# Kernel tuning notes

Hardware: AMD Instinct MI355X
Metric: run time of the kernel (lower is better)

Reference implementation:

```python
import jax, jax.numpy as jnp
import numpy as np

T, A, B, N = 16, 64, 64, 12
BATCH, ZS, ENC, DEC = 4096, 100, 400, 400


def setup_inputs() -> dict:
    key = jax.random.key(0)
    ks = jax.random.split(key, 20)
    s = 0.05  # small init so exp(log_sigma)/exp(log_delta) stay well-behaved
    rn = lambda k, shp: s * jax.random.normal(k, shp, dtype=jnp.float32)
    return {
        "x": jax.random.uniform(ks[0], (BATCH, A * B), dtype=jnp.float32),
        "eps": jax.random.normal(ks[1], (T, BATCH, ZS), dtype=jnp.float32),
        # encoder LSTMCell: input = read(2*N*N) concat h_dec(DEC)
        "w_enc_ih": rn(ks[2], (4 * ENC, 2 * N * N + DEC)),
        "w_enc_hh": rn(ks[3], (4 * ENC, ENC)),
        "b_enc_ih": jnp.zeros((4 * ENC,), jnp.float32),
        "b_enc_hh": jnp.zeros((4 * ENC,), jnp.float32),
        # decoder LSTMCell: input = z(ZS)
        "w_dec_ih": rn(ks[4], (4 * DEC, ZS)),
        "w_dec_hh": rn(ks[5], (4 * DEC, DEC)),
        "b_dec_ih": jnp.zeros((4 * DEC,), jnp.float32),
        "b_dec_hh": jnp.zeros((4 * DEC,), jnp.float32),
        "w_mu": rn(ks[6], (ZS, ENC)),
        "b_mu": jnp.zeros((ZS,), jnp.float32),
        "w_sig": rn(ks[7], (ZS, ENC)),
        "b_sig": jnp.zeros((ZS,), jnp.float32),
        "w_attn": rn(ks[8], (5, DEC)),
        "b_attn": jnp.zeros((5,), jnp.float32),
        "w_write": rn(ks[9], (N * N, DEC)),
        "b_write": jnp.zeros((N * N,), jnp.float32),
    }


def _lstm(inp, h, c, wi, wh, bi, bh):
    # PyTorch LSTMCell gate order: i, f, g, o
    g = inp @ wi.T + bi + h @ wh.T + bh
    i, f, gg, o = jnp.split(g, 4, axis=-1)
    c2 = jax.nn.sigmoid(f) * c + jax.nn.sigmoid(i) * jnp.tanh(gg)
    h2 = jax.nn.sigmoid(o) * jnp.tanh(c2)
    return h2, c2


def reference(x, eps, w_enc_ih, w_enc_hh, b_enc_ih, b_enc_hh,
              w_dec_ih, w_dec_hh, b_dec_ih, b_dec_hh,
              w_mu, b_mu, w_sig, b_sig, w_attn, b_attn, w_write, b_write):
    batch = x.shape[0]
    rng = jnp.arange(N, dtype=x.dtype)        # (N,)
    grid_a = jnp.arange(A, dtype=x.dtype)     # (A,)
    grid_b = jnp.arange(B, dtype=x.dtype)     # (B,)
    half = N / 2 + 0.5

    def attn(h_dec):
        p = h_dec @ w_attn.T + b_attn                       # (b,5)
        gx_, gy_, ls2, ld, lg = [p[:, i:i + 1] for i in range(5)]
        gx = (A + 1) / 2 * (gx_ + 1)
        gy = (B + 1) / 2 * (gy_ + 1)
        delta = (max(A, B) - 1) / (N - 1) * jnp.exp(ld)     # (b,1)
        sigma2 = jnp.exp(ls2)[:, :, None]                   # (b,1,1)
        gamma = jnp.exp(lg)                                  # (b,1)
        mu_x = (rng[None, :] - half) * delta + gx            # (b,N)
        mu_y = (rng[None, :] - half) * delta + gy

        def fb(grid, mu):
            t = (grid[None, None, :] - mu[:, :, None]) / (2 * sigma2)
            F = jnp.exp(-t * t)                              # (b,N,len)
            return F / (F.sum(2, keepdims=True) + 1e-9)
        return fb(grid_a, mu_x), fb(grid_b, mu_y), gamma

    def step(carry, eps_t):
        c, h_enc, s_enc, h_dec, s_dec = carry
        x_hat = x - jax.nn.sigmoid(c)
        Fx, Fy, gamma = attn(h_dec)

        def glimpse(img):  # Fy @ img @ Fx^T, scaled by gamma
            g = jnp.einsum('bnB,bBA,bmA->bnm', Fy, img.reshape(-1, B, A), Fx)
            return g.reshape(-1, N * N) * gamma

        r = jnp.concatenate([glimpse(x), glimpse(x_hat)], axis=1)  # (b,2*N*N)
        h_enc, s_enc = _lstm(jnp.concatenate([r, h_dec], axis=1),
                             h_enc, s_enc, w_enc_ih, w_enc_hh, b_enc_ih, b_enc_hh)
        mu = h_enc @ w_mu.T + b_mu
        logsig = h_enc @ w_sig.T + b_sig
        z = mu + jnp.exp(logsig) * eps_t
        h_dec, s_dec = _lstm(z, h_dec, s_dec, w_dec_ih, w_dec_hh, b_dec_ih, b_dec_hh)
        Fx2, Fy2, gamma2 = attn(h_dec)
        w = (h_dec @ w_write.T + b_write).reshape(-1, N, N)
        wr = jnp.einsum('bnB,bnm,bmA->bBA', Fy2, w, Fx2).reshape(-1, A * B) / gamma2
        return (c + wr, h_enc, s_enc, h_dec, s_dec), None

    zf = lambda d: jnp.zeros((batch, d), x.dtype)
    init = (jnp.zeros_like(x), zf(ENC), zf(ENC), zf(DEC), zf(DEC))
    (c, _, _, _, _), _ = jax.lax.scan(step, init, eps)
    return c  # final canvas logits, shape (batch, A*B)
```

## Files before the change

### kernel.cpp

```cpp
#include <hip/hip_runtime.h>
#include <cstdint>
#include <cstddef>

#define T_STEPS 16
#define AA 64
#define BBX 64
#define NF 12
#define BATCH 4096
#define ZS 100
#define ENC 400
#define DEC 400
#define IMG (AA*BBX)
#define RDIM (2*NF*NF)
#define GDIM (4*ENC)

#define KENC 1088
#define KDEC 544
#define KSML 416
#define NBIG 1664
#define NSML 256

typedef __attribute__((ext_vector_type(8))) short bfrag;
typedef __attribute__((ext_vector_type(4))) float f32x4;

__device__ __forceinline__ float sigmoidf_(float v) { return 1.f / (1.f + expf(-v)); }

__device__ __forceinline__ float bf2f(unsigned short u) {
    uint32_t x = ((uint32_t)u) << 16;
    return __builtin_bit_cast(float, x);
}

__device__ __forceinline__ void split2(float f, unsigned short& h, unsigned short& l) {
    uint32_t u = __builtin_bit_cast(uint32_t, f);
    uint32_t hb = (u + 0x7FFFu + ((u >> 16) & 1u)) >> 16;
    float hf = __builtin_bit_cast(float, hb << 16);
    float r = f - hf;
    uint32_t v = __builtin_bit_cast(uint32_t, r);
    uint32_t lb = (v + 0x7FFFu + ((v >> 16) & 1u)) >> 16;
    h = (unsigned short)hb;
    l = (unsigned short)lb;
}

__device__ __forceinline__ void bar_lds() {
    asm volatile("s_waitcnt lgkmcnt(0)" ::: "memory");
    __builtin_amdgcn_s_barrier();
    __builtin_amdgcn_sched_barrier(0);
}

__global__ __launch_bounds__(256, 2) void k_gemm2(
    const unsigned short* __restrict__ Ah, const unsigned short* __restrict__ Al,
    int lda, int a_off,
    const unsigned short* __restrict__ Bh, const unsigned short* __restrict__ Bl,
    int Kpad,
    const float* __restrict__ b1, const float* __restrict__ b2,
    float* __restrict__ C, int NN)
{
    __shared__ unsigned short lA[2][8 * 512];
    __shared__ unsigned short lB[2][8 * 512];

    const int tid = threadIdx.x;
    const int lane = tid & 63;
    const int wave = tid >> 6;
    const int wr = wave >> 1;
    const int wc = wave & 1;
    const int m0 = blockIdx.y * 128;
    const int n0 = blockIdx.x * 128;
    const int rlow = lane & 15;
    const int kg8 = (lane >> 4) * 8;

    const size_t aBase = (size_t)(m0 + rlow) * lda + a_off + kg8;
    const size_t bBase = (size_t)(n0 + rlow) * Kpad + kg8;
    const unsigned short* gsrc;
    unsigned short* ldst;
    size_t stride16;
    if (wave == 0)      { gsrc = Ah + aBase; ldst = &lA[0][0]; stride16 = (size_t)lda * 16; }
    else if (wave == 1) { gsrc = Al + aBase; ldst = &lA[1][0]; stride16 = (size_t)lda * 16; }
    else if (wave == 2) { gsrc = Bh + bBase; ldst = &lB[0][0]; stride16 = (size_t)Kpad * 16; }
    else                { gsrc = Bl + bBase; ldst = &lB[1][0]; stride16 = (size_t)Kpad * 16; }

    f32x4 acc[4][4];
#pragma unroll
    for (int mf = 0; mf < 4; ++mf)
#pragma unroll
        for (int nf = 0; nf < 4; ++nf) acc[mf][nf] = (f32x4){0.f, 0.f, 0.f, 0.f};

    for (int k0 = 0; k0 < Kpad; k0 += 32) {
#pragma unroll
        for (int sub = 0; sub < 8; ++sub) {
            __builtin_amdgcn_global_load_lds(
                (const __attribute__((address_space(1))) void*)(gsrc + (size_t)sub * stride16 + k0),
                (__attribute__((address_space(3))) void*)(ldst + sub * 512), 16, 0, 0);
        }
        __syncthreads();

        bfrag bhf[4], blf[4];
#pragma unroll
        for (int nf = 0; nf < 4; ++nf) {
            bhf[nf] = *(const bfrag*)&lB[0][(wc * 4 + nf) * 512 + lane * 8];
            blf[nf] = *(const bfrag*)&lB[1][(wc * 4 + nf) * 512 + lane * 8];
        }
#pragma unroll
        for (int mf = 0; mf < 4; ++mf) {
            const bfrag ah = *(const bfrag*)&lA[0][(wr * 4 + mf) * 512 + lane * 8];
            const bfrag al = *(const bfrag*)&lA[1][(wr * 4 + mf) * 512 + lane * 8];
#pragma unroll
            for (int nf = 0; nf < 4; ++nf) {
                acc[mf][nf] = __builtin_amdgcn_mfma_f32_16x16x32_bf16(ah, bhf[nf], acc[mf][nf], 0, 0, 0);
                acc[mf][nf] = __builtin_amdgcn_mfma_f32_16x16x32_bf16(ah, blf[nf], acc[mf][nf], 0, 0, 0);
                acc[mf][nf] = __builtin_amdgcn_mfma_f32_16x16x32_bf16(al, bhf[nf], acc[mf][nf], 0, 0, 0);
            }
        }
        __syncthreads();
    }

    const int col = lane & 15;
    const int rowq = (lane >> 4) * 4;
#pragma unroll
    for (int nf = 0; nf < 4; ++nf) {
        const int n = n0 + wc * 64 + nf * 16 + col;
        if (n < NN) {
            float bb = b1[n];
            if (b2) bb += b2[n];
#pragma unroll
            for (int mf = 0; mf < 4; ++mf) {
                const int mbase = m0 + wr * 64 + mf * 16 + rowq;
#pragma unroll
                for (int j = 0; j < 4; ++j)
                    C[(size_t)(mbase + j) * NN + n] = acc[mf][nf][j] + bb;
            }
        }
    }
}

__global__ __launch_bounds__(256) void k_fillw(
    const float* __restrict__ src, int rows, int cols,
    unsigned short* __restrict__ dh, unsigned short* __restrict__ dl,
    int ld, int col0, int row0)
{
    const int i = blockIdx.x * 256 + threadIdx.x;
    if (i >= rows * cols) return;
    const int r = i / cols, c = i - r * cols;
    unsigned short h, l;
    split2(src[i], h, l);
    dh[(size_t)(row0 + r) * ld + col0 + c] = h;
    dl[(size_t)(row0 + r) * ld + col0 + c] = l;
}

__device__ __forceinline__ void attn_compute(
    const float* __restrict__ hd,
    const float* __restrict__ w_attn, const float* __restrict__ b_attn,
    float* __restrict__ p,
    float (* __restrict__ Fx)[68], float (* __restrict__ Fy)[68],
    float* __restrict__ rowinv)
{
    const int t = threadIdx.x;
    const int lane = t & 63, wave = t >> 6;
    for (int o = wave; o < 5; o += 4) {
        float s = 0.f;
        for (int k = lane; k < DEC; k += 64) s += hd[k] * w_attn[o * DEC + k];
#pragma unroll
        for (int off = 32; off; off >>= 1) s += __shfl_down(s, off);
        if (lane == 0) p[o] = s + b_attn[o];
    }
    __syncthreads();
    const float gx = 32.5f * (p[0] + 1.f);
    const float gy = 32.5f * (p[1] + 1.f);
    const float sigma2 = expf(p[2]);
    const float delta = (63.f / 11.f) * expf(p[3]);
    const float inv2s = 1.f / (2.f * sigma2);
    for (int e = t; e < NF * 64; e += 256) {
        const int n = e >> 6, a = e & 63;
        const float mu_x = ((float)n - 6.5f) * delta + gx;
        const float mu_y = ((float)n - 6.5f) * delta + gy;
        const float tx = ((float)a - mu_x) * inv2s;
        const float ty = ((float)a - mu_y) * inv2s;
        Fx[n][a] = expf(-tx * tx);
        Fy[n][a] = expf(-ty * ty);
    }
    __syncthreads();
    for (int rix = wave; rix < 24; rix += 4) {
        const float* row = (rix < 12) ? &Fx[rix][0] : &Fy[rix - 12][0];
        float s = row[lane];
#pragma unroll
        for (int off = 32; off; off >>= 1) s += __shfl_down(s, off);
        if (lane == 0) rowinv[rix] = 1.f / (s + 1e-9f);
    }
    __syncthreads();
    for (int e = t; e < NF * 64; e += 256) {
        const int n = e >> 6, a = e & 63;
        Fx[n][a] *= rowinv[n];
        Fy[n][a] *= rowinv[12 + n];
    }
}

__global__ __launch_bounds__(256) void k_glimpse(
    const float* __restrict__ x, const float* __restrict__ c,
    unsigned short* __restrict__ eAh, unsigned short* __restrict__ eAl,
    const float* __restrict__ w_attn, const float* __restrict__ b_attn)
{
    __shared__ __align__(16) float hd[DEC];
    __shared__ __align__(16) float p[8];
    __shared__ __align__(16) float Fx[NF][68], Fy[NF][68];
    __shared__ __align__(16) float rowinv[24];
    __shared__ __align__(16) float img[IMG], imgh[IMG];
    __shared__ __align__(16) float tmp1[NF][68], tmp2[NF][68];
    const int item = blockIdx.x;
    const int t = threadIdx.x;
    const size_t arow = (size_t)item * KENC;

    for (int i = t; i < DEC; i += 256)
        hd[i] = bf2f(eAh[arow + 288 + i]) + bf2f(eAl[arow + 288 + i]);
    __syncthreads();
    attn_compute(hd, w_attn, b_attn, p, Fx, Fy, rowinv);

    for (int i = t; i < IMG; i += 256) {
        const float xv = x[(size_t)item * IMG + i];
        const float cv = c[(size_t)item * IMG + i];
        img[i] = xv;
        imgh[i] = xv - sigmoidf_(cv);
    }
    __syncthreads();
    const float gamma = expf(p[4]);

    if (t < 192) {
        const int n = t >> 4, a0 = (t & 15) * 4;
        float s10 = 0, s11 = 0, s12 = 0, s13 = 0;
        float s20 = 0, s21 = 0, s22 = 0, s23 = 0;
        for (int Bi = 0; Bi < 64; ++Bi) {
            const float fy = Fy[n][Bi];
            const float4 v1 = *(const float4*)&img[Bi * 64 + a0];
            const float4 v2 = *(const float4*)&imgh[Bi * 64 + a0];
            s10 += fy * v1.x; s11 += fy * v1.y; s12 += fy * v1.z; s13 += fy * v1.w;
            s20 += fy * v2.x; s21 += fy * v2.y; s22 += fy * v2.z; s23 += fy * v2.w;
        }
        *(float4*)&tmp1[n][a0] = make_float4(s10, s11, s12, s13);
        *(float4*)&tmp2[n][a0] = make_float4(s20, s21, s22, s23);
    }
    __syncthreads();

    for (int e = t; e < 2 * NF * NF; e += 256) {
        const int which = e / 144;
        const int idx = e - which * 144;
        const int n = idx / 12, m = idx - (idx / 12) * 12;
        const float (*tp)[68] = which ? tmp2 : tmp1;
        const float4* tv = (const float4*)&tp[n][0];
        const float4* fv = (const float4*)&Fx[m][0];
        float s = 0.f;
#pragma unroll
        for (int a4 = 0; a4 < 16; ++a4) {
            const float4 tvv = tv[a4], fvv = fv[a4];
            s += tvv.x * fvv.x + tvv.y * fvv.y + tvv.z * fvv.z + tvv.w * fvv.w;
        }
        unsigned short vh, vl;
        split2(s * gamma, vh, vl);
        eAh[arow + e] = vh;
        eAl[arow + e] = vl;
    }
}

__global__ __launch_bounds__(256) void k_wrgl(
    const float* __restrict__ x, float* __restrict__ c,
    unsigned short* __restrict__ eAh, unsigned short* __restrict__ eAl,
    const float* __restrict__ w_attn, const float* __restrict__ b_attn,
    const float* __restrict__ wvec)
{
    __shared__ __align__(16) float xx[64][64];
    __shared__ __align__(16) float gg[64][64];
    __shared__ __align__(16) float Fyf[16][68];
    __shared__ __align__(16) float Fx[NF][68];
    __shared__ __align__(16) float tmp[2][NF][68];
    __shared__ __align__(16) float u[64][13];
    __shared__ __align__(16) float hd[DEC];
    __shared__ __align__(16) float p[8];
    __shared__ __align__(16) float rowinv[24];
    __shared__ __align__(16) float wsv[NF * NF];
    const int item = blockIdx.x;
    const int t = threadIdx.x;
    const int lane = t & 63, wave = t >> 6;
    const size_t arow = (size_t)item * KENC;

    float4 cv4[4];
#pragma unroll
    for (int j = 0; j < 4; ++j)
        cv4[j] = *(const float4*)&c[(size_t)item * IMG + j * 1024 + t * 4];
    {
        const float* xsrc = x + (size_t)item * IMG + wave * 1024 + lane * 4;
        float* xdst = &xx[0][0] + wave * 1024;
#pragma unroll
        for (int j = 0; j < 4; ++j)
            __builtin_amdgcn_global_load_lds(
                (const __attribute__((address_space(1))) void*)(xsrc + j * 256),
                (__attribute__((address_space(3))) void*)(xdst + j * 256), 16, 0, 0);
    }
    {
        float hdv0 = bf2f(eAh[arow + 288 + t]) + bf2f(eAl[arow + 288 + t]);
        hd[t] = hdv0;
        if (t + 256 < DEC)
            hd[t + 256] = bf2f(eAh[arow + 288 + t + 256]) + bf2f(eAl[arow + 288 + t + 256]);
        if (t < NF * NF) wsv[t] = wvec[(size_t)item * (NF * NF) + t];
    }
    bar_lds();

    for (int o = wave; o < 5; o += 4) {
        float s = 0.f;
        for (int k = lane; k < DEC; k += 64) s += hd[k] * w_attn[o * DEC + k];
#pragma unroll
        for (int off = 32; off; off >>= 1) s += __shfl_down(s, off);
        if (lane == 0) p[o] = s + b_attn[o];
    }
    bar_lds();
    {
        const float gx = 32.5f * (p[0] + 1.f);
        const float gy = 32.5f * (p[1] + 1.f);
        const float sigma2 = expf(p[2]);
        const float delta = (63.f / 11.f) * expf(p[3]);
        const float inv2s = 1.f / (2.f * sigma2);
        for (int e = t; e < NF * 64; e += 256) {
            const int n = e >> 6, a = e & 63;
            const float mu_x = ((float)n - 6.5f) * delta + gx;
            const float mu_y = ((float)n - 6.5f) * delta + gy;
            const float tx = ((float)a - mu_x) * inv2s;
            const float ty = ((float)a - mu_y) * inv2s;
            Fx[n][a] = expf(-tx * tx);
            Fyf[n][a] = expf(-ty * ty);
        }
        for (int e = t; e < 4 * 68; e += 256)
            Fyf[12 + e / 68][e - (e / 68) * 68] = 0.f;
    }
    bar_lds();
    for (int rix = wave; rix < 24; rix += 4) {
        const float* row = (rix < 12) ? &Fx[rix][0] : &Fyf[rix - 12][0];
        float s = row[lane];
#pragma unroll
        for (int off = 32; off; off >>= 1) s += __shfl_down(s, off);
        if (lane == 0) rowinv[rix] = 1.f / (s + 1e-9f);
    }
    bar_lds();
    for (int e = t; e < NF * 64; e += 256) {
        const int n = e >> 6, a = e & 63;
        Fx[n][a] *= rowinv[n];
        Fyf[n][a] *= rowinv[12 + n];
    }
    bar_lds();
    const float gamma = expf(p[4]);
    const float ginv = 1.f / gamma;
    for (int e = t; e < 64 * NF; e += 256) {
        const int Bb = e / 12, m = e - (e / 12) * 12;
        float s = 0.f;
#pragma unroll
        for (int n = 0; n < 12; ++n) s += Fyf[n][Bb] * wsv[n * 12 + m];
        u[Bb][m] = s;
    }

    __syncthreads();
#pragma unroll
    for (int j = 0; j < 4; ++j) {
        const int i0 = j * 1024 + t * 4;
        const int Bb = i0 >> 6, a0 = i0 & 63;
        float s0 = 0, s1 = 0, s2 = 0, s3 = 0;
#pragma unroll
        for (int m = 0; m < 12; ++m) {
            const float um = u[Bb][m];
            s0 += um * Fx[m][a0];     s1 += um * Fx[m][a0 + 1];
            s2 += um * Fx[m][a0 + 2]; s3 += um * Fx[m][a0 + 3];
        }
        const float4 cn = make_float4(cv4[j].x + s0 * ginv, cv4[j].y + s1 * ginv,
                                      cv4[j].z + s2 * ginv, cv4[j].w + s3 * ginv);
        *(float4*)&c[(size_t)item * IMG + i0] = cn;
        const float4 xv = *(const float4*)&xx[Bb][a0];
        *(float4*)&gg[Bb][a0] = make_float4(
            xv.x - sigmoidf_(cn.x), xv.y - sigmoidf_(cn.y),
            xv.z - sigmoidf_(cn.z), xv.w - sigmoidf_(cn.w));
    }
    bar_lds();

    {
        const int at = wave;
        const int arow16 = at * 16 + (lane & 15);
        const int nrow = lane & 15;
        const int kb0 = (lane >> 4) * 8;
        f32x4 acc1 = (f32x4){0.f, 0.f, 0.f, 0.f};
        f32x4 acc2 = (f32x4){0.f, 0.f, 0.f, 0.f};
#pragma unroll
        for (int ksub = 0; ksub < 2; ++ksub) {
            const int kb = ksub * 32 + kb0;
            bfrag fh, fl, xh, xl, gh, gl;
#pragma unroll
            for (int e = 0; e < 8; ++e) {
                unsigned short h, l;
                split2(Fyf[nrow][kb + e], h, l); fh[e] = (short)h; fl[e] = (short)l;
                split2(xx[kb + e][arow16], h, l); xh[e] = (short)h; xl[e] = (short)l;
                split2(gg[kb + e][arow16], h, l); gh[e] = (short)h; gl[e] = (short)l;
            }
            acc1 = __builtin_amdgcn_mfma_f32_16x16x32_bf16(fh, xh, acc1, 0, 0, 0);
            acc1 = __builtin_amdgcn_mfma_f32_16x16x32_bf16(fh, xl, acc1, 0, 0, 0);
            acc1 = __builtin_amdgcn_mfma_f32_16x16x32_bf16(fl, xh, acc1, 0, 0, 0);
            acc2 = __builtin_amdgcn_mfma_f32_16x16x32_bf16(fh, gh, acc2, 0, 0, 0);
            acc2 = __builtin_amdgcn_mfma_f32_16x16x32_bf16(fh, gl, acc2, 0, 0, 0);
            acc2 = __builtin_amdgcn_mfma_f32_16x16x32_bf16(fl, gh, acc2, 0, 0, 0);
        }
        const int acol = at * 16 + (lane & 15);
#pragma unroll
        for (int j = 0; j < 4; ++j) {
            const int n = (lane >> 4) * 4 + j;
            if (n < 12) {
                tmp[0][n][acol] = acc1[j];
                tmp[1][n][acol] = acc2[j];
            }
        }
    }
    bar_lds();

    for (int e = t; e < 2 * NF * NF; e += 256) {
        const int which = e / 144;
        const int idx = e - which * 144;
        const int n = idx / 12, m = idx - (idx / 12) * 12;
        const float4* tv = (const float4*)&tmp[which][n][0];
        const float4* fv = (const float4*)&Fx[m][0];
        float s = 0.f;
#pragma unroll
        for (int a4 = 0; a4 < 16; ++a4) {
            const float4 tvv = tv[a4], fvv = fv[a4];
            s += tvv.x * fvv.x + tvv.y * fvv.y + tvv.z * fvv.z + tvv.w * fvv.w;
        }
        unsigned short vh, vl;
        split2(s * gamma, vh, vl);
        eAh[arow + e] = vh;
        eAl[arow + e] = vl;
    }
}

__global__ __launch_bounds__(256) void k_lstm(
    const float* __restrict__ gates, float* __restrict__ s,
    unsigned short* __restrict__ d1h, unsigned short* __restrict__ d1l, int ld1,
    unsigned short* __restrict__ d2h, unsigned short* __restrict__ d2l, int ld2)
{
    const int idx = blockIdx.x * 256 + threadIdx.x;
    if (idx >= BATCH * ENC) return;
    const int m = idx / ENC, n = idx - m * ENC;
    const float* g = gates + (size_t)m * GDIM;
    const float gi = g[n], gf = g[n + 400], gg = g[n + 800], go = g[n + 1200];
    const float cold = s[idx];
    const float c2 = sigmoidf_(gf) * cold + sigmoidf_(gi) * tanhf(gg);
    s[idx] = c2;
    const float h = sigmoidf_(go) * tanhf(c2);
    unsigned short hh, hl;
    split2(h, hh, hl);
    d1h[(size_t)m * ld1 + n] = hh;
    d1l[(size_t)m * ld1 + n] = hl;
    if (d2h) {
        d2h[(size_t)m * ld2 + n] = hh;
        d2l[(size_t)m * ld2 + n] = hl;
    }
}

__global__ __launch_bounds__(256) void k_zelem(
    const float* __restrict__ mus, const float* __restrict__ eps_t,
    unsigned short* __restrict__ dzh, unsigned short* __restrict__ dzl)
{
    const int idx = blockIdx.x * 256 + threadIdx.x;
    if (idx >= BATCH * ZS) return;
    const int m = idx / ZS, o = idx - m * ZS;
    const float zv = mus[(size_t)m * 200 + o] + expf(mus[(size_t)m * 200 + 100 + o]) * eps_t[idx];
    unsigned short h, l;
    split2(zv, h, l);
    dzh[(size_t)m * KDEC + o] = h;
    dzl[(size_t)m * KDEC + o] = l;
}

__global__ __launch_bounds__(256) void k_write(
    const unsigned short* __restrict__ eAh, const unsigned short* __restrict__ eAl,
    const float* __restrict__ w_attn, const float* __restrict__ b_attn,
    const float* __restrict__ wvec,
    float* __restrict__ c)
{
    __shared__ __align__(16) float hd[DEC];
    __shared__ __align__(16) float p[8];
    __shared__ __align__(16) float Fx[NF][68], Fy[NF][68];
    __shared__ __align__(16) float rowinv[24];
    __shared__ __align__(16) float wsv[NF * NF];
    __shared__ __align__(16) float u[64][13];
    const int item = blockIdx.x;
    const int t = threadIdx.x;
    const size_t arow = (size_t)item * KENC;

    for (int i = t; i < DEC; i += 256)
        hd[i] = bf2f(eAh[arow + 288 + i]) + bf2f(eAl[arow + 288 + i]);
    if (t < NF * NF) wsv[t] = wvec[(size_t)item * (NF * NF) + t];
    __syncthreads();
    attn_compute(hd, w_attn, b_attn, p, Fx, Fy, rowinv);
    __syncthreads();
    const float ginv = 1.f / expf(p[4]);

    for (int e = t; e < 64 * NF; e += 256) {
        const int Bb = e / 12, m = e - (e / 12) * 12;
        float s = 0.f;
#pragma unroll
        for (int n = 0; n < 12; ++n) s += Fy[n][Bb] * wsv[n * 12 + m];
        u[Bb][m] = s;
    }
    __syncthreads();
    for (int i = t; i < IMG; i += 256) {
        const int Bb = i >> 6, a = i & 63;
        float s = 0.f;
#pragma unroll
        for (int m = 0; m < 12; ++m) s += u[Bb][m] * Fx[m][a];
        c[(size_t)item * IMG + i] += s * ginv;
    }
}

extern "C" void kernel_launch(void* const* d_in, const int* in_sizes, int n_in,
                              void* d_out, int out_size, void* d_ws, size_t ws_size,
                              hipStream_t stream)
{
    const float* x        = (const float*)d_in[0];
    const float* eps      = (const float*)d_in[1];
    const float* w_enc_ih = (const float*)d_in[2];
    const float* w_enc_hh = (const float*)d_in[3];
    const float* b_enc_ih = (const float*)d_in[4];
    const float* b_enc_hh = (const float*)d_in[5];
    const float* w_dec_ih = (const float*)d_in[6];
    const float* w_dec_hh = (const float*)d_in[7];
    const float* b_dec_ih = (const float*)d_in[8];
    const float* b_dec_hh = (const float*)d_in[9];
    const float* w_mu     = (const float*)d_in[10];
    const float* b_mu     = (const float*)d_in[11];
    const float* w_sig    = (const float*)d_in[12];
    const float* b_sig    = (const float*)d_in[13];
    const float* w_attn   = (const float*)d_in[14];
    const float* b_attn   = (const float*)d_in[15];
    const float* w_write  = (const float*)d_in[16];
    const float* b_write  = (const float*)d_in[17];

    float* canvas = (float*)d_out;

    uint8_t* p = (uint8_t*)d_ws;
    auto nextu = [&](size_t elems) {
        unsigned short* r = (unsigned short*)p;
        p += (elems * 2 + 255) & ~(size_t)255;
        return r;
    };
    auto nextf = [&](size_t elems) {
        float* r = (float*)p;
        p += (elems * 4 + 255) & ~(size_t)255;
        return r;
    };
    uint8_t* zstart = p;
    unsigned short* encA_h = nextu((size_t)(BATCH + 1) * KENC);
    unsigned short* encA_l = nextu((size_t)(BATCH + 1) * KENC);
    unsigned short* decA_h = nextu((size_t)(BATCH + 1) * KDEC);
    unsigned short* decA_l = nextu((size_t)(BATCH + 1) * KDEC);
    unsigned short* encB_h = nextu((size_t)NBIG * KENC);
    unsigned short* encB_l = nextu((size_t)NBIG * KENC);
    unsigned short* decB_h = nextu((size_t)NBIG * KDEC);
    unsigned short* decB_l = nextu((size_t)NBIG * KDEC);
    unsigned short* musB_h = nextu((size_t)NSML * KSML);
    unsigned short* musB_l = nextu((size_t)NSML * KSML);
    unsigned short* wrtB_h = nextu((size_t)NSML * KSML);
    unsigned short* wrtB_l = nextu((size_t)NSML * KSML);
    float* s_enc = nextf((size_t)BATCH * ENC);
    float* s_dec = nextf((size_t)BATCH * DEC);
    float* b_cat = nextf(256);
    uint8_t* zend = p;
    float* gates = nextf((size_t)BATCH * GDIM);
    float* mus   = nextf((size_t)BATCH * 200);
    float* wvec  = nextf((size_t)BATCH * (NF * NF));

    hipMemsetAsync(zstart, 0, (size_t)(zend - zstart), stream);
    hipMemsetAsync(canvas, 0, (size_t)BATCH * IMG * sizeof(float), stream);

    auto fill = [&](const float* src, int rows, int cols,
                    unsigned short* dh, unsigned short* dl, int ld, int col0, int row0) {
        k_fillw<<<dim3((rows * cols + 255) / 256), 256, 0, stream>>>(
            src, rows, cols, dh, dl, ld, col0, row0);
    };
    fill(w_enc_ih, 1600, 688, encB_h, encB_l, KENC, 0, 0);
    fill(w_enc_hh, 1600, 400, encB_h, encB_l, KENC, 688, 0);
    fill(w_dec_ih, 1600, 100, decB_h, decB_l, KDEC, 0, 0);
    fill(w_dec_hh, 1600, 400, decB_h, decB_l, KDEC, 128, 0);
    fill(w_mu,     100, 400, musB_h, musB_l, KSML, 0, 0);
    fill(w_sig,    100, 400, musB_h, musB_l, KSML, 0, 100);
    fill(w_write,  144, 400, wrtB_h, wrtB_l, KSML, 0, 0);
    hipMemcpyAsync(b_cat,       b_mu,  100 * 4, hipMemcpyDeviceToDevice, stream);
    hipMemcpyAsync(b_cat + 100, b_sig, 100 * 4, hipMemcpyDeviceToDevice, stream);

    const dim3 blk(256);
    k_glimpse<<<BATCH, blk, 0, stream>>>(x, canvas, encA_h, encA_l, w_attn, b_attn);
    for (int t = 0; t < T_STEPS; ++t) {
        k_gemm2<<<dim3(13, 32), blk, 0, stream>>>(encA_h, encA_l, KENC, 0,
            encB_h, encB_l, KENC, b_enc_ih, b_enc_hh, gates, GDIM);
        k_lstm<<<dim3((BATCH * ENC + 255) / 256), blk, 0, stream>>>(gates, s_enc,
            encA_h + 688, encA_l + 688, KENC, nullptr, nullptr, 0);
        k_gemm2<<<dim3(2, 32), blk, 0, stream>>>(encA_h, encA_l, KENC, 688,
            musB_h, musB_l, KSML, b_cat, nullptr, mus, 200);
        k_zelem<<<dim3((BATCH * ZS + 255) / 256), blk, 0, stream>>>(
            mus, eps + (size_t)t * BATCH * ZS, decA_h, decA_l);
        k_gemm2<<<dim3(13, 32), blk, 0, stream>>>(decA_h, decA_l, KDEC, 0,
            decB_h, decB_l, KDEC, b_dec_ih, b_dec_hh, gates, GDIM);
        k_lstm<<<dim3((BATCH * ENC + 255) / 256), blk, 0, stream>>>(gates, s_dec,
            encA_h + 288, encA_l + 288, KENC, decA_h + 128, decA_l + 128, KDEC);
        k_gemm2<<<dim3(2, 32), blk, 0, stream>>>(encA_h, encA_l, KENC, 288,
            wrtB_h, wrtB_l, KSML, b_write, nullptr, wvec, NF * NF);
        if (t < T_STEPS - 1) {
            k_wrgl<<<BATCH, blk, 0, stream>>>(x, canvas, encA_h, encA_l,
                                              w_attn, b_attn, wvec);
        } else {
            k_write<<<BATCH, blk, 0, stream>>>(encA_h, encA_l, w_attn, b_attn,
                                               wvec, canvas);
        }
    }
}
```

Before: 4.595 ms.

## Fuse LSTM gate GEMM with cell update using interleaved gate weights and ping-pong hidden buffers

Adds k_gemm_lstm, which permutes the LSTM weight rows so that the four gates of each unit sit in adjacent columns. The GEMM epilogue can then apply the cell/hidden update directly through shared memory, so the fp32 gates buffer and the separate k_lstm pass go away. Hidden states now live in double-buffered split-bf16 arrays, so a block can read h while others write the new h, and the A operand is taken from two source pointers. k_wrgl moves to 512 threads and replaces the MFMA-based Fy contraction with a scalar fp32 loop. In return the epilogue is more complex and needs extra syncthreads.

Result: faster. 4.014 ms (-12.6%).

```diff
diff --git a/kernel.cpp b/kernel.cpp
--- a/kernel.cpp
+++ b/kernel.cpp
@@ -3,20 +3,19 @@
 #include <cstddef>
 
 #define T_STEPS 16
-#define AA 64
-#define BBX 64
 #define NF 12
 #define BATCH 4096
 #define ZS 100
 #define ENC 400
 #define DEC 400
-#define IMG (AA*BBX)
-#define RDIM (2*NF*NF)
-#define GDIM (4*ENC)
-
-#define KENC 1088
-#define KDEC 544
-#define KSML 416
+#define IMG 4096
+#define GDIM 1600
+
+#define KEA 704
+#define KEB 1120
+#define KDA 128
+#define KDB 544
+#define KH  416
 #define NBIG 1664
 #define NSML 256
 
@@ -61,8 +60,7 @@
     const int tid = threadIdx.x;
     const int lane = tid & 63;
     const int wave = tid >> 6;
-    const int wr = wave >> 1;
-    const int wc = wave & 1;
+    const int wr = wave >> 1, wc = wave & 1;
     const int m0 = blockIdx.y * 128;
     const int n0 = blockIdx.x * 128;
     const int rlow = lane & 15;
@@ -92,7 +90,6 @@
                 (__attribute__((address_space(3))) void*)(ldst + sub * 512), 16, 0, 0);
         }
         __syncthreads();
-
         bfrag bhf[4], blf[4];
 #pragma unroll
         for (int nf = 0; nf < 4; ++nf) {
@@ -132,18 +129,152 @@
     }
 }
 
+__global__ __launch_bounds__(256, 2) void k_gemm_lstm(
+    const unsigned short* __restrict__ A0h, const unsigned short* __restrict__ A0l,
+    int lda0, int KS0,
+    const unsigned short* __restrict__ A1h, const unsigned short* __restrict__ A1l,
+    int lda1,
+    const unsigned short* __restrict__ Bh, const unsigned short* __restrict__ Bl,
+    int Kpad,
+    const float* __restrict__ b1, const float* __restrict__ b2,
+    float* __restrict__ s,
+    unsigned short* __restrict__ d1h, unsigned short* __restrict__ d1l, int ld1,
+    unsigned short* __restrict__ d2h, unsigned short* __restrict__ d2l, int ld2)
+{
+    __shared__ __align__(16) uint8_t smem[33792];
+    unsigned short* lA0 = (unsigned short*)smem;
+    unsigned short* lA1 = lA0 + 4096;
+    unsigned short* lB0 = (unsigned short*)(smem + 16384);
+    unsigned short* lB1 = lB0 + 4096;
+
+    const int tid = threadIdx.x;
+    const int lane = tid & 63;
+    const int wave = tid >> 6;
+    const int wr = wave >> 1, wc = wave & 1;
+    const int m0 = blockIdx.y * 128;
+    const int n0 = blockIdx.x * 128;
+    const int u0 = blockIdx.x * 32;
+    const int rlow = lane & 15;
+    const int kg8 = (lane >> 4) * 8;
+    const int col = lane & 15;
+    const int rowq = (lane >> 4) * 4;
+
+    const unsigned short* pA0;
+    const unsigned short* pA1;
+    const unsigned short* pB;
+    unsigned short* ldst;
+    if (wave == 0)      { pA0 = A0h + (size_t)(m0 + rlow) * lda0 + kg8;
+                          pA1 = A1h + (size_t)(m0 + rlow) * lda1 + kg8; ldst = lA0; pB = nullptr; }
+    else if (wave == 1) { pA0 = A0l + (size_t)(m0 + rlow) * lda0 + kg8;
+                          pA1 = A1l + (size_t)(m0 + rlow) * lda1 + kg8; ldst = lA1; pB = nullptr; }
+    else if (wave == 2) { pB = Bh + (size_t)(n0 + rlow) * Kpad + kg8; ldst = lB0; pA0 = pA1 = nullptr; }
+    else                { pB = Bl + (size_t)(n0 + rlow) * Kpad + kg8; ldst = lB1; pA0 = pA1 = nullptr; }
+    const size_t sA0 = (size_t)lda0 * 16, sA1 = (size_t)lda1 * 16, sB = (size_t)Kpad * 16;
+
+    f32x4 acc[4][4];
+#pragma unroll
+    for (int mf = 0; mf < 4; ++mf)
+#pragma unroll
+        for (int nf = 0; nf < 4; ++nf) acc[mf][nf] = (f32x4){0.f, 0.f, 0.f, 0.f};
+
+    for (int k0 = 0; k0 < Kpad; k0 += 32) {
+        if (wave < 2) {
+            const unsigned short* src = (k0 < KS0) ? (pA0 + k0) : (pA1 + (k0 - KS0));
+            const size_t st = (k0 < KS0) ? sA0 : sA1;
+#pragma unroll
+            for (int sub = 0; sub < 8; ++sub)
+                __builtin_amdgcn_global_load_lds(
+                    (const __attribute__((address_space(1))) void*)(src + (size_t)sub * st),
+                    (__attribute__((address_space(3))) void*)(ldst + sub * 512), 16, 0, 0);
+        } else {
+#pragma unroll
+            for (int sub = 0; sub < 8; ++sub)
+                __builtin_amdgcn_global_load_lds(
+                    (const __attribute__((address_space(1))) void*)(pB + k0 + (size_t)sub * sB),
+                    (__attribute__((address_space(3))) void*)(ldst + sub * 512), 16, 0, 0);
+        }
+        __syncthreads();
+        bfrag bhf[4], blf[4];
+#pragma unroll
+        for (int nf = 0; nf < 4; ++nf) {
+            bhf[nf] = *(const bfrag*)&lB0[(wc * 4 + nf) * 512 + lane * 8];
+            blf[nf] = *(const bfrag*)&lB1[(wc * 4 + nf) * 512 + lane * 8];
+        }
+#pragma unroll
+        for (int mf = 0; mf < 4; ++mf) {
+            const bfrag ah = *(const bfrag*)&lA0[(wr * 4 + mf) * 512 + lane * 8];
+            const bfrag al = *(const bfrag*)&lA1[(wr * 4 + mf) * 512 + lane * 8];
+#pragma unroll
+            for (int nf = 0; nf < 4; ++nf) {
+                acc[mf][nf] = __builtin_amdgcn_mfma_f32_16x16x32_bf16(ah, bhf[nf], acc[mf][nf], 0, 0, 0);
+                acc[mf][nf] = __builtin_amdgcn_mfma_f32_16x16x32_bf16(ah, blf[nf], acc[mf][nf], 0, 0, 0);
+                acc[mf][nf] = __builtin_amdgcn_mfma_f32_16x16x32_bf16(al, bhf[nf], acc[mf][nf], 0, 0, 0);
+            }
+        }
+        __syncthreads();
+    }
+
+    float bb[4];
+#pragma unroll
+    for (int nf = 0; nf < 4; ++nf) {
+        const int np = n0 + wc * 64 + nf * 16 + col;
+        const int g = np & 3, uu = np >> 2;
+        bb[nf] = (uu < 400) ? (b1[g * 400 + uu] + b2[g * 400 + uu]) : 0.f;
+    }
+    float (*gt)[132] = (float (*)[132])smem;
+    const int u_l = lane & 31;
+    const int ug = u0 + u_l;
+    const int mo = lane >> 5;
+
+#pragma unroll
+    for (int h = 0; h < 2; ++h) {
+        if (wr == h) {
+#pragma unroll
+            for (int mf = 0; mf < 4; ++mf)
+#pragma unroll
+                for (int nf = 0; nf < 4; ++nf)
+#pragma unroll
+                    for (int j = 0; j < 4; ++j)
+                        gt[mf * 16 + rowq + j][wc * 64 + nf * 16 + col] = acc[mf][nf][j] + bb[nf];
+        }
+        __syncthreads();
+        if (ug < 400) {
+#pragma unroll
+            for (int i = 0; i < 8; ++i) {
+                const int ml = mo * 32 + wave * 8 + i;
+                const size_t row = (size_t)(m0 + h * 64 + ml);
+                const f32x4 g4 = *(const f32x4*)&gt[ml][u_l * 4];
+                const float cold = s[row * 400 + ug];
+                const float c2 = sigmoidf_(g4[1]) * cold + sigmoidf_(g4[0]) * tanhf(g4[2]);
+                s[row * 400 + ug] = c2;
+                const float hv = sigmoidf_(g4[3]) * tanhf(c2);
+                unsigned short hh, hl;
+                split2(hv, hh, hl);
+                d1h[row * ld1 + ug] = hh;
+                d1l[row * ld1 + ug] = hl;
+                if (d2h) {
+                    d2h[row * ld2 + ug] = hh;
+                    d2l[row * ld2 + ug] = hl;
+                }
+            }
+        }
+        __syncthreads();
+    }
+}
+
 __global__ __launch_bounds__(256) void k_fillw(
     const float* __restrict__ src, int rows, int cols,
     unsigned short* __restrict__ dh, unsigned short* __restrict__ dl,
-    int ld, int col0, int row0)
+    int ld, int col0, int row0, int gperm)
 {
     const int i = blockIdx.x * 256 + threadIdx.x;
     if (i >= rows * cols) return;
     const int r = i / cols, c = i - r * cols;
+    const int rr = gperm ? ((r % 400) * 4 + r / 400) : r;
     unsigned short h, l;
     split2(src[i], h, l);
-    dh[(size_t)(row0 + r) * ld + col0 + c] = h;
-    dl[(size_t)(row0 + r) * ld + col0 + c] = l;
+    dh[(size_t)(row0 + rr) * ld + col0 + c] = h;
+    dl[(size_t)(row0 + rr) * ld + col0 + c] = l;
 }
 
 __device__ __forceinline__ void attn_compute(
@@ -206,7 +337,7 @@
     __shared__ __align__(16) float tmp1[NF][68], tmp2[NF][68];
     const int item = blockIdx.x;
     const int t = threadIdx.x;
-    const size_t arow = (size_t)item * KENC;
+    const size_t arow = (size_t)item * KEA;
 
     for (int i = t; i < DEC; i += 256)
         hd[i] = bf2f(eAh[arow + 288 + i]) + bf2f(eAl[arow + 288 + i]);
@@ -258,7 +389,7 @@
     }
 }
 
-__global__ __launch_bounds__(256) void k_wrgl(
+__global__ __launch_bounds__(512) void k_wrgl(
     const float* __restrict__ x, float* __restrict__ c,
     unsigned short* __restrict__ eAh, unsigned short* __restrict__ eAl,
     const float* __restrict__ w_attn, const float* __restrict__ b_attn,
@@ -266,42 +397,36 @@
 {
     __shared__ __align__(16) float xx[64][64];
     __shared__ __align__(16) float gg[64][64];
-    __shared__ __align__(16) float Fyf[16][68];
-    __shared__ __align__(16) float Fx[NF][68];
-    __shared__ __align__(16) float tmp[2][NF][68];
-    __shared__ __align__(16) float u[64][13];
     __shared__ __align__(16) float hd[DEC];
     __shared__ __align__(16) float p[8];
+    __shared__ __align__(16) float Fx[NF][68], Fy[NF][68];
     __shared__ __align__(16) float rowinv[24];
     __shared__ __align__(16) float wsv[NF * NF];
+    __shared__ __align__(16) float u[64][13];
+    __shared__ __align__(16) float tmp[2][NF][68];
     const int item = blockIdx.x;
     const int t = threadIdx.x;
     const int lane = t & 63, wave = t >> 6;
-    const size_t arow = (size_t)item * KENC;
-
-    float4 cv4[4];
-#pragma unroll
-    for (int j = 0; j < 4; ++j)
-        cv4[j] = *(const float4*)&c[(size_t)item * IMG + j * 1024 + t * 4];
+    const size_t arow = (size_t)item * KEA;
+
+    float4 cv4[2];
+#pragma unroll
+    for (int j = 0; j < 2; ++j)
+        cv4[j] = *(const float4*)&c[(size_t)item * IMG + j * 2048 + t * 4];
     {
-        const float* xsrc = x + (size_t)item * IMG + wave * 1024 + lane * 4;
-        float* xdst = &xx[0][0] + wave * 1024;
-#pragma unroll
-        for (int j = 0; j < 4; ++j)
+        const float* xsrc = x + (size_t)item * IMG + wave * 512 + lane * 4;
+        float* xdst = &xx[0][0] + wave * 512;
+#pragma unroll
+        for (int j = 0; j < 2; ++j)
             __builtin_amdgcn_global_load_lds(
                 (const __attribute__((address_space(1))) void*)(xsrc + j * 256),
                 (__attribute__((address_space(3))) void*)(xdst + j * 256), 16, 0, 0);
     }
-    {
-        float hdv0 = bf2f(eAh[arow + 288 + t]) + bf2f(eAl[arow + 288 + t]);
-        hd[t] = hdv0;
-        if (t + 256 < DEC)
-            hd[t + 256] = bf2f(eAh[arow + 288 + t + 256]) + bf2f(eAl[arow + 288 + t + 256]);
-        if (t < NF * NF) wsv[t] = wvec[(size_t)item * (NF * NF) + t];
-    }
+    if (t < DEC) hd[t] = bf2f(eAh[arow + 288 + t]) + bf2f(eAl[arow + 288 + t]);
+    if (t < NF * NF) wsv[t] = wvec[(size_t)item * (NF * NF) + t];
     bar_lds();
 
-    for (int o = wave; o < 5; o += 4) {
+    for (int o = wave; o < 5; o += 8) {
         float s = 0.f;
         for (int k = lane; k < DEC; k += 64) s += hd[k] * w_attn[o * DEC + k];
 #pragma unroll
@@ -315,47 +440,45 @@
         const float sigma2 = expf(p[2]);
         const float delta = (63.f / 11.f) * expf(p[3]);
         const float inv2s = 1.f / (2.f * sigma2);
-        for (int e = t; e < NF * 64; e += 256) {
+        for (int e = t; e < NF * 64; e += 512) {
             const int n = e >> 6, a = e & 63;
             const float mu_x = ((float)n - 6.5f) * delta + gx;
             const float mu_y = ((float)n - 6.5f) * delta + gy;
             const float tx = ((float)a - mu_x) * inv2s;
             const float ty = ((float)a - mu_y) * inv2s;
             Fx[n][a] = expf(-tx * tx);
-            Fyf[n][a] = expf(-ty * ty);
-        }
-        for (int e = t; e < 4 * 68; e += 256)
-            Fyf[12 + e / 68][e - (e / 68) * 68] = 0.f;
+            Fy[n][a] = expf(-ty * ty);
+        }
     }
     bar_lds();
-    for (int rix = wave; rix < 24; rix += 4) {
-        const float* row = (rix < 12) ? &Fx[rix][0] : &Fyf[rix - 12][0];
+    for (int rix = wave; rix < 24; rix += 8) {
+        const float* row = (rix < 12) ? &Fx[rix][0] : &Fy[rix - 12][0];
         float s = row[lane];
 #pragma unroll
         for (int off = 32; off; off >>= 1) s += __shfl_down(s, off);
         if (lane == 0) rowinv[rix] = 1.f / (s + 1e-9f);
     }
     bar_lds();
-    for (int e = t; e < NF * 64; e += 256) {
+    for (int e = t; e < NF * 64; e += 512) {
         const int n = e >> 6, a = e & 63;
         Fx[n][a] *= rowinv[n];
-        Fyf[n][a] *= rowinv[12 + n];
+        Fy[n][a] *= rowinv[12 + n];
     }
     bar_lds();
     const float gamma = expf(p[4]);
     const float ginv = 1.f / gamma;
-    for (int e = t; e < 64 * NF; e += 256) {
+    for (int e = t; e < 64 * NF; e += 512) {
         const int Bb = e / 12, m = e - (e / 12) * 12;
         float s = 0.f;
 #pragma unroll
-        for (int n = 0; n < 12; ++n) s += Fyf[n][Bb] * wsv[n * 12 + m];
+        for (int n = 0; n < 12; ++n) s += Fy[n][Bb] * wsv[n * 12 + m];
         u[Bb][m] = s;
     }
 
     __syncthreads();
 #pragma unroll
-    for (int j = 0; j < 4; ++j) {
-        const int i0 = j * 1024 + t * 4;
+    for (int j = 0; j < 2; ++j) {
+        const int i0 = j * 2048 + t * 4;
         const int Bb = i0 >> 6, a0 = i0 & 63;
         float s0 = 0, s1 = 0, s2 = 0, s3 = 0;
 #pragma unroll
@@ -374,46 +497,24 @@
     }
     bar_lds();
 
-    {
-        const int at = wave;
-        const int arow16 = at * 16 + (lane & 15);
-        const int nrow = lane & 15;
-        const int kb0 = (lane >> 4) * 8;
-        f32x4 acc1 = (f32x4){0.f, 0.f, 0.f, 0.f};
-        f32x4 acc2 = (f32x4){0.f, 0.f, 0.f, 0.f};
-#pragma unroll
-        for (int ksub = 0; ksub < 2; ++ksub) {
-            const int kb = ksub * 32 + kb0;
-            bfrag fh, fl, xh, xl, gh, gl;
-#pragma unroll
-            for (int e = 0; e < 8; ++e) {
-                unsigned short h, l;
-                split2(Fyf[nrow][kb + e], h, l); fh[e] = (short)h; fl[e] = (short)l;
-                split2(xx[kb + e][arow16], h, l); xh[e] = (short)h; xl[e] = (short)l;
-                split2(gg[kb + e][arow16], h, l); gh[e] = (short)h; gl[e] = (short)l;
-            }
-            acc1 = __builtin_amdgcn_mfma_f32_16x16x32_bf16(fh, xh, acc1, 0, 0, 0);
-            acc1 = __builtin_amdgcn_mfma_f32_16x16x32_bf16(fh, xl, acc1, 0, 0, 0);
-            acc1 = __builtin_amdgcn_mfma_f32_16x16x32_bf16(fl, xh, acc1, 0, 0, 0);
-            acc2 = __builtin_amdgcn_mfma_f32_16x16x32_bf16(fh, gh, acc2, 0, 0, 0);
-            acc2 = __builtin_amdgcn_mfma_f32_16x16x32_bf16(fh, gl, acc2, 0, 0, 0);
-            acc2 = __builtin_amdgcn_mfma_f32_16x16x32_bf16(fl, gh, acc2, 0, 0, 0);
-        }
-        const int acol = at * 16 + (lane & 15);
-#pragma unroll
-        for (int j = 0; j < 4; ++j) {
-            const int n = (lane >> 4) * 4 + j;
-            if (n < 12) {
-                tmp[0][n][acol] = acc1[j];
-                tmp[1][n][acol] = acc2[j];
-            }
-        }
+    if (t < 384) {
+        const int which = t / 192;
+        const int r2 = t - which * 192;
+        const int n = r2 >> 4, a0 = (r2 & 15) * 4;
+        const float (*src)[64] = which ? gg : xx;
+        float s0 = 0, s1 = 0, s2 = 0, s3 = 0;
+        for (int Bi = 0; Bi < 64; ++Bi) {
+            const float fy = Fy[n][Bi];
+            const float4 v = *(const float4*)&src[Bi][a0];
+            s0 += fy * v.x; s1 += fy * v.y; s2 += fy * v.z; s3 += fy * v.w;
+        }
+        *(float4*)&tmp[which][n][a0] = make_float4(s0, s1, s2, s3);
     }
     bar_lds();
 
-    for (int e = t; e < 2 * NF * NF; e += 256) {
-        const int which = e / 144;
-        const int idx = e - which * 144;
+    if (t < 2 * NF * NF) {
+        const int which = t / 144;
+        const int idx = t - which * 144;
         const int n = idx / 12, m = idx - (idx / 12) * 12;
         const float4* tv = (const float4*)&tmp[which][n][0];
         const float4* fv = (const float4*)&Fx[m][0];
@@ -425,32 +526,8 @@
         }
         unsigned short vh, vl;
         split2(s * gamma, vh, vl);
-        eAh[arow + e] = vh;
-        eAl[arow + e] = vl;
-    }
-}
-
-__global__ __launch_bounds__(256) void k_lstm(
-    const float* __restrict__ gates, float* __restrict__ s,
-    unsigned short* __restrict__ d1h, unsigned short* __restrict__ d1l, int ld1,
-    unsigned short* __restrict__ d2h, unsigned short* __restrict__ d2l, int ld2)
-{
-    const int idx = blockIdx.x * 256 + threadIdx.x;
-    if (idx >= BATCH * ENC) return;
-    const int m = idx / ENC, n = idx - m * ENC;
-    const float* g = gates + (size_t)m * GDIM;
-    const float gi = g[n], gf = g[n + 400], gg = g[n + 800], go = g[n + 1200];
-    const float cold = s[idx];
-    const float c2 = sigmoidf_(gf) * cold + sigmoidf_(gi) * tanhf(gg);
-    s[idx] = c2;
-    const float h = sigmoidf_(go) * tanhf(c2);
-    unsigned short hh, hl;
-    split2(h, hh, hl);
-    d1h[(size_t)m * ld1 + n] = hh;
-    d1l[(size_t)m * ld1 + n] = hl;
-    if (d2h) {
-        d2h[(size_t)m * ld2 + n] = hh;
-        d2l[(size_t)m * ld2 + n] = hl;
+        eAh[arow + t] = vh;
+        eAl[arow + t] = vl;
     }
 }
 
@@ -464,8 +541,8 @@
     const float zv = mus[(size_t)m * 200 + o] + expf(mus[(size_t)m * 200 + 100 + o]) * eps_t[idx];
     unsigned short h, l;
     split2(zv, h, l);
-    dzh[(size_t)m * KDEC + o] = h;
-    dzl[(size_t)m * KDEC + o] = l;
+    dzh[(size_t)m * KDA + o] = h;
+    dzl[(size_t)m * KDA + o] = l;
 }
 
 __global__ __launch_bounds__(256) void k_write(
@@ -482,7 +559,7 @@
     __shared__ __align__(16) float u[64][13];
     const int item = blockIdx.x;
     const int t = threadIdx.x;
-    const size_t arow = (size_t)item * KENC;
+    const size_t arow = (size_t)item * KEA;
 
     for (int i = t; i < DEC; i += 256)
         hd[i] = bf2f(eAh[arow + 288 + i]) + bf2f(eAl[arow + 288 + i]);
@@ -546,23 +623,29 @@
         return r;
     };
     uint8_t* zstart = p;
-    unsigned short* encA_h = nextu((size_t)(BATCH + 1) * KENC);
-    unsigned short* encA_l = nextu((size_t)(BATCH + 1) * KENC);
-    unsigned short* decA_h = nextu((size_t)(BATCH + 1) * KDEC);
-    unsigned short* decA_l = nextu((size_t)(BATCH + 1) * KDEC);
-    unsigned short* encB_h = nextu((size_t)NBIG * KENC);
-    unsigned short* encB_l = nextu((size_t)NBIG * KENC);
-    unsigned short* decB_h = nextu((size_t)NBIG * KDEC);
-    unsigned short* decB_l = nextu((size_t)NBIG * KDEC);
-    unsigned short* musB_h = nextu((size_t)NSML * KSML);
-    unsigned short* musB_l = nextu((size_t)NSML * KSML);
-    unsigned short* wrtB_h = nextu((size_t)NSML * KSML);
-    unsigned short* wrtB_l = nextu((size_t)NSML * KSML);
+    unsigned short* encA_h = nextu((size_t)(BATCH + 1) * KEA);
+    unsigned short* encA_l = nextu((size_t)(BATCH + 1) * KEA);
+    unsigned short* decA_h = nextu((size_t)(BATCH + 1) * KDA);
+    unsigned short* decA_l = nextu((size_t)(BATCH + 1) * KDA);
+    unsigned short* hencH[2], *hencL[2], *hdecH[2], *hdecL[2];
+    for (int i = 0; i < 2; ++i) {
+        hencH[i] = nextu((size_t)(BATCH + 1) * KH);
+        hencL[i] = nextu((size_t)(BATCH + 1) * KH);
+        hdecH[i] = nextu((size_t)(BATCH + 1) * KH);
+        hdecL[i] = nextu((size_t)(BATCH + 1) * KH);
+    }
+    unsigned short* encB_h = nextu((size_t)NBIG * KEB);
+    unsigned short* encB_l = nextu((size_t)NBIG * KEB);
+    unsigned short* decB_h = nextu((size_t)NBIG * KDB);
+    unsigned short* decB_l = nextu((size_t)NBIG * KDB);
+    unsigned short* musB_h = nextu((size_t)NSML * KH);
+    unsigned short* musB_l = nextu((size_t)NSML * KH);
+    unsigned short* wrtB_h = nextu((size_t)NSML * KH);
+    unsigned short* wrtB_l = nextu((size_t)NSML * KH);
     float* s_enc = nextf((size_t)BATCH * ENC);
     float* s_dec = nextf((size_t)BATCH * DEC);
     float* b_cat = nextf(256);
     uint8_t* zend = p;
-    float* gates = nextf((size_t)BATCH * GDIM);
     float* mus   = nextf((size_t)BATCH * 200);
     float* wvec  = nextf((size_t)BATCH * (NF * NF));
 
@@ -570,42 +653,43 @@
     hipMemsetAsync(canvas, 0, (size_t)BATCH * IMG * sizeof(float), stream);
 
     auto fill = [&](const float* src, int rows, int cols,
-                    unsigned short* dh, unsigned short* dl, int ld, int col0, int row0) {
+                    unsigned short* dh, unsigned short* dl, int ld, int col0,
+                    int row0, int gperm) {
         k_fillw<<<dim3((rows * cols + 255) / 256), 256, 0, stream>>>(
-            src, rows, cols, dh, dl, ld, col0, row0);
+            src, rows, cols, dh, dl, ld, col0, row0, gperm);
     };
-    fill(w_enc_ih, 1600, 688, encB_h, encB_l, KENC, 0, 0);
-    fill(w_enc_hh, 1600, 400, encB_h, encB_l, KENC, 688, 0);
-    fill(w_dec_ih, 1600, 100, decB_h, decB_l, KDEC, 0, 0);
-    fill(w_dec_hh, 1600, 400, decB_h, decB_l, KDEC, 128, 0);
-    fill(w_mu,     100, 400, musB_h, musB_l, KSML, 0, 0);
-    fill(w_sig,    100, 400, musB_h, musB_l, KSML, 0, 100);
-    fill(w_write,  144, 400, wrtB_h, wrtB_l, KSML, 0, 0);
+    fill(w_enc_ih, 1600, 688, encB_h, encB_l, KEB, 0,   0,   1);
+    fill(w_enc_hh, 1600, 400, encB_h, encB_l, KEB, 704, 0,   1);
+    fill(w_dec_ih, 1600, 100, decB_h, decB_l, KDB, 0,   0,   1);
+    fill(w_dec_hh, 1600, 400, decB_h, decB_l, KDB, 128, 0,   1);
+    fill(w_mu,     100, 400, musB_h, musB_l, KH,  0,   0,   0);
+    fill(w_sig,    100, 400, musB_h, musB_l, KH,  0,   100, 0);
+    fill(w_write,  144, 400, wrtB_h, wrtB_l, KH,  0,   0,   0);
     hipMemcpyAsync(b_cat,       b_mu,  100 * 4, hipMemcpyDeviceToDevice, stream);
     hipMemcpyAsync(b_cat + 100, b_sig, 100 * 4, hipMemcpyDeviceToDevice, stream);
 
-    const dim3 blk(256);
-    k_glimpse<<<BATCH, blk, 0, stream>>>(x, canvas, encA_h, encA_l, w_attn, b_attn);
+    k_glimpse<<<BATCH, 256, 0, stream>>>(x, canvas, encA_h, encA_l, w_attn, b_attn);
     for (int t = 0; t < T_STEPS; ++t) {
-        k_gemm2<<<dim3(13, 32), blk, 0, stream>>>(encA_h, encA_l, KENC, 0,
-            encB_h, encB_l, KENC, b_enc_ih, b_enc_hh, gates, GDIM);
-        k_lstm<<<dim3((BATCH * ENC + 255) / 256), blk, 0, stream>>>(gates, s_enc,
-            encA_h + 688, encA_l + 688, KENC, nullptr, nullptr, 0);
-        k_gemm2<<<dim3(2, 32), blk, 0, stream>>>(encA_h, encA_l, KENC, 688,
-            musB_h, musB_l, KSML, b_cat, nullptr, mus, 200);
-        k_zelem<<<dim3((BATCH * ZS + 255) / 256), blk, 0, stream>>>(
+        const int cur = t & 1, nxt = cur ^ 1;
+        k_gemm_lstm<<<dim3(13, 32), 256, 0, stream>>>(
+            encA_h, encA_l, KEA, 704, hencH[cur], hencL[cur], KH,
+            encB_h, encB_l, KEB, b_enc_ih, b_enc_hh, s_enc,
+            hencH[nxt], hencL[nxt], KH, nullptr, nullptr, 0);
+        k_gemm2<<<dim3(2, 32), 256, 0, stream>>>(hencH[nxt], hencL[nxt], KH, 0,
+            musB_h, musB_l, KH, b_cat, nullptr, mus, 200);
+        k_zelem<<<dim3((BATCH * ZS + 255) / 256), 256, 0, stream>>>(
             mus, eps + (size_t)t * BATCH * ZS, decA_h, decA_l);
-        k_gemm2<<<dim3(13, 32), blk, 0, stream>>>(decA_h, decA_l, KDEC, 0,
-            decB_h, decB_l, KDEC, b_dec_ih, b_dec_hh, gates, GDIM);
-        k_lstm<<<dim3((BATCH * ENC + 255) / 256), blk, 0, stream>>>(gates, s_dec,
-            encA_h + 288, encA_l + 288, KENC, decA_h + 128, decA_l + 128, KDEC);
-        k_gemm2<<<dim3(2, 32), blk, 0, stream>>>(encA_h, encA_l, KENC, 288,
-            wrtB_h, wrtB_l, KSML, b_write, nullptr, wvec, NF * NF);
+        k_gemm_lstm<<<dim3(13, 32), 256, 0, stream>>>(
+            decA_h, decA_l, KDA, 128, hdecH[cur], hdecL[cur], KH,
+            decB_h, decB_l, KDB, b_dec_ih, b_dec_hh, s_dec,
+            encA_h + 288, encA_l + 288, KEA, hdecH[nxt], hdecL[nxt], KH);
+        k_gemm2<<<dim3(2, 32), 256, 0, stream>>>(encA_h, encA_l, KEA, 288,
+            wrtB_h, wrtB_l, KH, b_write, nullptr, wvec, NF * NF);
         if (t < T_STEPS - 1) {
-            k_wrgl<<<BATCH, blk, 0, stream>>>(x, canvas, encA_h, encA_l,
+            k_wrgl<<<BATCH, 512, 0, stream>>>(x, canvas, encA_h, encA_l,
                                               w_attn, b_attn, wvec);
         } else {
-            k_write<<<BATCH, blk, 0, stream>>>(encA_h, encA_l, w_attn, b_attn,
+            k_write<<<BATCH, 256, 0, stream>>>(encA_h, encA_l, w_attn, b_attn,
                                                wvec, canvas);
         }
     }
```
